# Performance work log

Measured on AMD Instinct MI355X. Metric: run time of the kernel, lower is better.

The kernel has to match this reference:

```python
import jax, jax.numpy as jnp
import numpy as np

N_NODES = 50000
N_EDGES = 600000
N_GRAPHS = 500


def gcn_conv(x, src, dst, W, b, n_nodes):
    # PyG GCNConv: add self-loops, symmetric normalization D^-1/2 (A+I) D^-1/2, then XW + b
    h = x @ W  # [N, F_out]
    loop = jnp.arange(n_nodes)
    s = jnp.concatenate([src, loop])
    d = jnp.concatenate([dst, loop])
    deg = jax.ops.segment_sum(jnp.ones_like(d, dtype=h.dtype), d, num_segments=n_nodes)
    dinv = jnp.where(deg > 0, jax.lax.rsqrt(jnp.maximum(deg, 1.0)), 0.0)
    norm = dinv[s] * dinv[d]  # [E+N]
    msg = h[s] * norm[:, None]  # gather + scale
    out = jax.ops.segment_sum(msg, d, num_segments=n_nodes)  # scatter-add
    return out + b


def setup_inputs() -> dict:
    key = jax.random.key(0)
    ks = jax.random.split(key, 12)
    F_in, H, Hf, D_out = 128, 128, 64, 1
    x = jax.random.normal(ks[0], (N_NODES, F_in), dtype=jnp.float32)
    edge_index = jax.random.randint(ks[1], (2, N_EDGES), 0, N_NODES, dtype=jnp.int64)
    batch = jnp.sort(jax.random.randint(ks[2], (N_NODES,), 0, N_GRAPHS, dtype=jnp.int64))
    def glorot(k, shape):
        lim = np.sqrt(6.0 / (shape[0] + shape[1]))
        return jax.random.uniform(k, shape, jnp.float32, -lim, lim)
    return {
        "x": x, "edge_index": edge_index, "batch": batch,
        "W1": glorot(ks[3], (F_in, H)), "b1": jnp.zeros((H,), jnp.float32),
        "W2": glorot(ks[4], (H, H)), "b2": jnp.zeros((H,), jnp.float32),
        "W3": glorot(ks[5], (H, H)), "b3": jnp.zeros((H,), jnp.float32),
        "Wf1": glorot(ks[6], (H, Hf)), "bf1": jnp.zeros((Hf,), jnp.float32),
        "Wf2": glorot(ks[7], (Hf, D_out)), "bf2": jnp.zeros((D_out,), jnp.float32),
    }


def reference(x, edge_index, batch, W1, b1, W2, b2, W3, b3, Wf1, bf1, Wf2, bf2):
    src, dst = edge_index[0], edge_index[1]
    n = x.shape[0]
    h = jax.nn.relu(gcn_conv(x, src, dst, W1, b1, n))
    h = jax.nn.relu(gcn_conv(h, src, dst, W2, b2, n))
    h = jax.nn.relu(gcn_conv(h, src, dst, W3, b3, n))
    # global_mean_pool: segment mean over graphs
    sums = jax.ops.segment_sum(h, batch, num_segments=N_GRAPHS)
    cnts = jax.ops.segment_sum(jnp.ones((n,), h.dtype), batch, num_segments=N_GRAPHS)
    hg = sums / jnp.maximum(cnts, 1.0)[:, None]  # [G, 128]
    h = jax.nn.relu(hg @ Wf1 + bf1)
    return h @ Wf2 + bf2
```

## Files before the change

### kernel.cpp

```cpp
#include <hip/hip_runtime.h>

#define N_NODES 50000
#define N_EDGES 600000
#define N_GRAPHS 500
#define F 128

typedef short bf16x8 __attribute__((ext_vector_type(8)));
typedef float f32x4 __attribute__((ext_vector_type(4)));
union U4H8 { uint4 u; bf16x8 h; };

__device__ inline unsigned pk_bf16(float a, float b) {
    unsigned ua = __float_as_uint(a), ub = __float_as_uint(b);
    ua = (ua + 0x7fffu + ((ua >> 16) & 1u)) >> 16;
    ub = (ub + 0x7fffu + ((ub >> 16) & 1u)) >> 16;
    return ua | (ub << 16);
}
__device__ inline float bf16_rnd(float x) {
    unsigned u = __float_as_uint(x);
    u = (u + 0x7fffu + ((u >> 16) & 1u)) & 0xffff0000u;
    return __uint_as_float(u);
}
__device__ inline unsigned short bf16_1(float a) {
    unsigned ua = __float_as_uint(a);
    return (unsigned short)((ua + 0x7fffu + ((ua >> 16) & 1u)) >> 16);
}
#define BF_LO(u) __uint_as_float((u) << 16)
#define BF_HI(u) __uint_as_float((u) & 0xffff0000u)

#define G_CVT  3125
#define G_HIST 2344
#define G_PREPW 24
#define G_BND  196

__global__ __launch_bounds__(256) void k_prep(const float* __restrict__ x, unsigned short* __restrict__ xb,
                                              const int* __restrict__ dst, int* __restrict__ cnt,
                                              int* __restrict__ rnk,
                                              const float* __restrict__ W1, const float* __restrict__ W2,
                                              const float* __restrict__ W3,
                                              uint4* __restrict__ Whi, uint4* __restrict__ Wlo,
                                              const int* __restrict__ batch, int* __restrict__ gs) {
    int b = blockIdx.x, tid = threadIdx.x;
    if (b < G_CVT) {
        int idx = b * 256 + tid;
        if (idx < N_NODES * F / 8) {
            const float4* xr = (const float4*)(x + (size_t)idx * 8);
            float4 a = xr[0], c = xr[1];
            uint4 o;
            o.x = pk_bf16(a.x, a.y); o.y = pk_bf16(a.z, a.w);
            o.z = pk_bf16(c.x, c.y); o.w = pk_bf16(c.z, c.w);
            ((uint4*)xb)[idx] = o;
        }
    } else if (b < G_CVT + G_HIST) {
        int e = (b - G_CVT) * 256 + tid;
        if (e < N_EDGES) rnk[e] = atomicAdd(&cnt[dst[e]], 1);
    } else if (b < G_CVT + G_HIST + G_PREPW) {
        int idx = (b - G_CVT - G_HIST) * 256 + tid;
        int layer = idx >> 11;
        const float* W = (layer == 0) ? W1 : (layer == 1) ? W2 : W3;
        int t = idx & 2047;
        int lane = t & 63, sc = t >> 6;
        int s = sc >> 3, c = sc & 7;
        int q = lane >> 4, m = lane & 15;
        int k0 = 32 * s + 8 * q, n0 = 16 * c + m;
        float w[8], h[8];
        #pragma unroll
        for (int j = 0; j < 8; ++j) {
            w[j] = W[(k0 + j) * F + n0];
            h[j] = bf16_rnd(w[j]);
        }
        uint4 uh, ul;
        uh.x = pk_bf16(h[0], h[1]); uh.y = pk_bf16(h[2], h[3]);
        uh.z = pk_bf16(h[4], h[5]); uh.w = pk_bf16(h[6], h[7]);
        ul.x = pk_bf16(w[0] - h[0], w[1] - h[1]); ul.y = pk_bf16(w[2] - h[2], w[3] - h[3]);
        ul.z = pk_bf16(w[4] - h[4], w[5] - h[5]); ul.w = pk_bf16(w[6] - h[6], w[7] - h[7]);
        Whi[idx] = uh;
        Wlo[idx] = ul;
    } else {
        int i = (b - G_CVT - G_HIST - G_PREPW) * 256 + tid;
        if (i < N_NODES) {
            int bi = batch[i];
            if (i == 0) {
                for (int g = 0; g <= bi; ++g) gs[g] = 0;
            } else {
                int bp = batch[i - 1];
                for (int g = bp + 1; g <= bi; ++g) gs[g] = i;
            }
            if (i == N_NODES - 1) {
                for (int g = bi + 1; g <= N_GRAPHS; ++g) gs[g] = N_NODES;
            }
        }
    }
}

__global__ __launch_bounds__(256) void k_scan1(const int* __restrict__ cnt, int* __restrict__ row_ptr,
                                               int* __restrict__ blksums, float* __restrict__ dinv,
                                               int* __restrict__ dh, int n) {
    __shared__ int s[256];
    __shared__ int dhl[64];
    int tid = threadIdx.x;
    int i = blockIdx.x * 256 + tid;
    if (tid < 64) dhl[tid] = 0;
    int v = (i < n) ? cnt[i] : 0;
    if (i < n) dinv[i] = rsqrtf((float)(v + 1));
    s[tid] = v;
    __syncthreads();
    if (i < n) atomicAdd(&dhl[v < 63 ? v : 63], 1);
    for (int off = 1; off < 256; off <<= 1) {
        int t = (tid >= off) ? s[tid - off] : 0;
        __syncthreads();
        s[tid] += t;
        __syncthreads();
    }
    if (i < n) row_ptr[i] = s[tid] - v;
    if (tid == 255) blksums[blockIdx.x] = s[255];
    __syncthreads();
    if (tid < 64 && dhl[tid] > 0) atomicAdd(&dh[tid], dhl[tid]);
}

__global__ __launch_bounds__(256) void k_scan23(int* __restrict__ row_ptr, const int* __restrict__ blksums,
                                                const int* __restrict__ dh, int* __restrict__ dhoff,
                                                int* __restrict__ dcur, int n, int ne) {
    __shared__ int s[256];
    int tid = threadIdx.x;
    s[tid] = (tid < (int)blockIdx.x) ? blksums[tid] : 0;
    __syncthreads();
    for (int off = 128; off > 0; off >>= 1) {
        if (tid < off) s[tid] += s[tid + off];
        __syncthreads();
    }
    int base = s[0];
    int i = blockIdx.x * 256 + tid;
    if (i < n) row_ptr[i] += base;
    if (i == 0) row_ptr[n] = ne;
    if (blockIdx.x == 0 && tid < 64) {
        int v = dh[tid];
        int x = v;
        #pragma unroll
        for (int off = 1; off < 64; off <<= 1) {
            int t = __shfl_up(x, off, 64);
            if (tid >= off) x += t;
        }
        dhoff[tid] = x - v;
        dcur[tid] = 0;
    }
}

#define G_FILL 2344
#define G_PLACE 196
__global__ __launch_bounds__(256) void k_fill(const int* __restrict__ src, const int* __restrict__ dst,
                                              const int* __restrict__ row_ptr, const int* __restrict__ rnk,
                                              int* __restrict__ esrc,
                                              const int* __restrict__ dhoff, int* __restrict__ dcur,
                                              int* __restrict__ perm, int ne) {
    __shared__ int lh[64];
    __shared__ int lbase[64];
    int b = blockIdx.x, tid = threadIdx.x;
    if (b < G_FILL) {
        int e = b * 256 + tid;
        if (e < ne) {
            int d = dst[e];
            esrc[row_ptr[d] + rnk[e]] = src[e];
        }
    } else {
        int i = (b - G_FILL) * 256 + tid;
        if (tid < 64) lh[tid] = 0;
        __syncthreads();
        int deg = 0, rank = 0;
        bool valid = (i < N_NODES);
        if (valid) {
            deg = row_ptr[i + 1] - row_ptr[i];
            if (deg > 63) deg = 63;
            rank = atomicAdd(&lh[deg], 1);
        }
        __syncthreads();
        if (tid < 64 && lh[tid] > 0)
            lbase[tid] = atomicAdd(&dcur[tid], lh[tid]);
        __syncthreads();
        if (valid) perm[dhoff[deg] + lbase[deg] + rank] = i;
    }
}

#define TN 32
#define GP2 136
#define CAPG 32
__global__ __launch_bounds__(256) void k_fused(const int* __restrict__ row_ptr,
                                               const int* __restrict__ esrc,
                                               const float* __restrict__ dinv,
                                               const int* __restrict__ perm,
                                               const unsigned short* __restrict__ Hin,
                                               const uint4* __restrict__ Whi,
                                               const uint4* __restrict__ Wlo,
                                               const float* __restrict__ bias,
                                               unsigned short* __restrict__ Hout, int n) {
    __shared__ unsigned short Gb[TN * GP2];
    __shared__ uint2 eLg[TN][CAPG];
    __shared__ int nodeL[TN], begL[TN], endL[TN];
    __shared__ float ddl[TN];
    int tid = threadIdx.x;
    int d0 = blockIdx.x * TN;
    int grp = tid >> 4, sub = tid & 15;

    if (tid < TN) {
        int slot = d0 + tid;
        int node = (slot < n) ? perm[slot] : -1;
        nodeL[tid] = node;
        if (node >= 0) {
            begL[tid] = row_ptr[node];
            endL[tid] = row_ptr[node + 1];
            ddl[tid] = dinv[node];
        } else {
            begL[tid] = 0; endL[tid] = 0; ddl[tid] = 0.f;
        }
    }
    __syncthreads();

    #pragma unroll 1
    for (int n2 = 0; n2 < 2; ++n2) {
        int gi = grp + 16 * n2;
        int node = nodeL[gi];
        int beg = begL[gi], end = endL[gi];
        int deg = end - beg;
        float dd = ddl[gi];

        int degc = deg < CAPG ? deg : CAPG;
        for (int i = sub; i < degc; i += 16) {
            int s = esrc[beg + i];
            eLg[gi][i] = make_uint2((unsigned)s, (unsigned)__float_as_int(dinv[s]));
        }

        float4 accL = make_float4(0.f, 0.f, 0.f, 0.f);
        float4 accH = make_float4(0.f, 0.f, 0.f, 0.f);
        if (node >= 0) {
            uint4 srow = ((const uint4*)(Hin + (size_t)node * F))[sub];
            float ws = dd * dd;
            accL.x = BF_LO(srow.x) * ws;
            accL.y = BF_HI(srow.x) * ws;
            accL.z = BF_LO(srow.y) * ws;
            accL.w = BF_HI(srow.y) * ws;
            accH.x = BF_LO(srow.z) * ws;
            accH.y = BF_HI(srow.z) * ws;
            accH.z = BF_LO(srow.w) * ws;
            accH.w = BF_HI(srow.w) * ws;
            for (int c = 0; c < deg; c += 8) {
                int sjs[8];
                #pragma unroll
                for (int j = 0; j < 8; ++j) {
                    int e = c + j;
                    int sj = node;
                    if (e < deg) sj = (e < CAPG) ? (int)eLg[gi][e].x
                                                 : esrc[beg + e];
                    sjs[j] = sj;
                }
                uint4 rows[8];
                #pragma unroll
                for (int j = 0; j < 8; ++j)
                    rows[j] = ((const uint4*)(Hin + (size_t)sjs[j] * F))[sub];
                #pragma unroll
                for (int j = 0; j < 8; ++j) {
                    int e = c + j;
                    float wj = 0.f;
                    if (e < deg) {
                        float dv = (e < CAPG) ? __uint_as_float(eLg[gi][e].y)
                                              : dinv[sjs[j]];
                        wj = dv * dd;
                    }
                    accL.x = fmaf(BF_LO(rows[j].x), wj, accL.x);
                    accL.y = fmaf(BF_HI(rows[j].x), wj, accL.y);
                    accL.z = fmaf(BF_LO(rows[j].y), wj, accL.z);
                    accL.w = fmaf(BF_HI(rows[j].y), wj, accL.w);
                    accH.x = fmaf(BF_LO(rows[j].z), wj, accH.x);
                    accH.y = fmaf(BF_HI(rows[j].z), wj, accH.y);
                    accH.z = fmaf(BF_LO(rows[j].w), wj, accH.z);
                    accH.w = fmaf(BF_HI(rows[j].w), wj, accH.w);
                }
            }
        }
        {
            uint4 o;
            o.x = pk_bf16(accL.x, accL.y);
            o.y = pk_bf16(accL.z, accL.w);
            o.z = pk_bf16(accH.x, accH.y);
            o.w = pk_bf16(accH.z, accH.w);
            *(uint4*)&Gb[gi * GP2 + 8 * sub] = o;
        }
    }
    __syncthreads();

    int wave = tid >> 6, lane = tid & 63;
    int q = lane >> 4, m = lane & 15;
    f32x4 acc0[2], acc1[2];
    acc0[0] = (f32x4){0.f, 0.f, 0.f, 0.f};
    acc0[1] = (f32x4){0.f, 0.f, 0.f, 0.f};
    acc1[0] = (f32x4){0.f, 0.f, 0.f, 0.f};
    acc1[1] = (f32x4){0.f, 0.f, 0.f, 0.f};
    #pragma unroll
    for (int s = 0; s < 4; ++s) {
        U4H8 a0, a1;
        a0.u = *(const uint4*)&Gb[m * GP2 + 32 * s + 8 * q];
        a1.u = *(const uint4*)&Gb[(m + 16) * GP2 + 32 * s + 8 * q];
        #pragma unroll
        for (int cc = 0; cc < 2; ++cc) {
            int c = wave * 2 + cc;
            U4H8 bh, bl;
            bh.u = Whi[(s * 8 + c) * 64 + lane];
            bl.u = Wlo[(s * 8 + c) * 64 + lane];
            acc0[cc] = __builtin_amdgcn_mfma_f32_16x16x32_bf16(a0.h, bh.h, acc0[cc], 0, 0, 0);
            acc0[cc] = __builtin_amdgcn_mfma_f32_16x16x32_bf16(a0.h, bl.h, acc0[cc], 0, 0, 0);
            acc1[cc] = __builtin_amdgcn_mfma_f32_16x16x32_bf16(a1.h, bh.h, acc1[cc], 0, 0, 0);
            acc1[cc] = __builtin_amdgcn_mfma_f32_16x16x32_bf16(a1.h, bl.h, acc1[cc], 0, 0, 0);
        }
    }
    __syncthreads();

    #pragma unroll
    for (int cc = 0; cc < 2; ++cc) {
        int c = wave * 2 + cc;
        float bb = bias[16 * c + m];
        #pragma unroll
        for (int r = 0; r < 4; ++r) {
            Gb[(4 * q + r) * GP2 + 16 * c + m] = bf16_1(fmaxf(acc0[cc][r] + bb, 0.f));
            Gb[(16 + 4 * q + r) * GP2 + 16 * c + m] = bf16_1(fmaxf(acc1[cc][r] + bb, 0.f));
        }
    }
    __syncthreads();
    {
        int row = tid >> 4, c8 = tid & 15;
        #pragma unroll
        for (int rr = 0; rr < 2; ++rr) {
            int r2 = row + 16 * rr;
            int onode = nodeL[r2];
            if (onode >= 0) {
                uint4 o = *(const uint4*)&Gb[r2 * GP2 + c8 * 8];
                ((uint4*)(Hout + (size_t)onode * F))[c8] = o;
            }
        }
    }
}

__global__ __launch_bounds__(256) void k_pool_fc(const unsigned short* __restrict__ Hb,
                                                 const int* __restrict__ gs,
                                                 const float* __restrict__ Wf1,
                                                 const float* __restrict__ bf1,
                                                 const float* __restrict__ Wf2,
                                                 const float* __restrict__ bf2,
                                                 float* __restrict__ out) {
    int g = blockIdx.x;
    int tid = threadIdx.x;
    int start = gs[g], end = gs[g + 1];

    __shared__ float hs[4][F];
    __shared__ float hg[F];
    int wv = tid >> 6, lane = tid & 63;
    int half = lane >> 5, sub = lane & 31;
    float4 a = make_float4(0.f, 0.f, 0.f, 0.f);
    for (int i = start + wv * 2 + half; i < end; i += 8) {
        uint2 v = ((const uint2*)(Hb + (size_t)i * F))[sub];
        a.x += BF_LO(v.x); a.y += BF_HI(v.x);
        a.z += BF_LO(v.y); a.w += BF_HI(v.y);
    }
    a.x += __shfl_xor(a.x, 32, 64);
    a.y += __shfl_xor(a.y, 32, 64);
    a.z += __shfl_xor(a.z, 32, 64);
    a.w += __shfl_xor(a.w, 32, 64);
    if (half == 0) ((float4*)hs[wv])[sub] = a;
    __syncthreads();
    if (tid < F) {
        float inv = 1.0f / (float)((end - start) > 0 ? (end - start) : 1);
        hg[tid] = (hs[0][tid] + hs[1][tid] + hs[2][tid] + hs[3][tid]) * inv;
    }
    __syncthreads();
    if (tid < 64) {
        float acc = bf1[tid];
        #pragma unroll 4
        for (int f = 0; f < F; ++f) acc = fmaf(hg[f], Wf1[f * 64 + tid], acc);
        float v = fmaxf(acc, 0.f) * Wf2[tid];
        #pragma unroll
        for (int off = 32; off > 0; off >>= 1) v += __shfl_down(v, off, 64);
        if (tid == 0) out[g] = v + bf2[0];
    }
}

extern "C" void kernel_launch(void* const* d_in, const int* in_sizes, int n_in,
                              void* d_out, int out_size, void* d_ws, size_t ws_size,
                              hipStream_t stream) {
    const float* x    = (const float*)d_in[0];
    const int* eidx   = (const int*)d_in[1];
    const int* batch  = (const int*)d_in[2];
    const float* W1   = (const float*)d_in[3];
    const float* b1   = (const float*)d_in[4];
    const float* W2   = (const float*)d_in[5];
    const float* b2   = (const float*)d_in[6];
    const float* W3   = (const float*)d_in[7];
    const float* b3   = (const float*)d_in[8];
    const float* Wf1  = (const float*)d_in[9];
    const float* bf1  = (const float*)d_in[10];
    const float* Wf2  = (const float*)d_in[11];
    const float* bf2  = (const float*)d_in[12];
    float* out = (float*)d_out;

    const int* src = eidx;
    const int* dst = eidx + N_EDGES;

    char* p = (char*)d_ws;
    unsigned short* Xb  = (unsigned short*)p;  p += (size_t)N_NODES * F * 2;
    unsigned short* H1  = (unsigned short*)p;  p += (size_t)N_NODES * F * 2;
    unsigned short* H2  = (unsigned short*)p;  p += (size_t)N_NODES * F * 2;
    unsigned short* H3  = (unsigned short*)p;  p += (size_t)N_NODES * F * 2;
    int* esrc   = (int*)p;     p += (size_t)N_EDGES * sizeof(int);
    int* rnk    = (int*)p;     p += (size_t)N_EDGES * sizeof(int);
    uint4* Whi  = (uint4*)p;   p += (size_t)3 * 2048 * sizeof(uint4);
    uint4* Wlo  = (uint4*)p;   p += (size_t)3 * 2048 * sizeof(uint4);
    float* dinv = (float*)p;   p += (size_t)N_NODES * sizeof(float);
    int* cnt     = (int*)p;    p += (size_t)N_NODES * sizeof(int);
    int* dh      = (int*)p;    p += 64 * sizeof(int);
    int* row_ptr = (int*)p;    p += (size_t)(N_NODES + 1) * sizeof(int);
    int* blksums = (int*)p;    p += 256 * sizeof(int);
    int* gs      = (int*)p;    p += (size_t)(N_GRAPHS + 1) * sizeof(int);
    int* dhoff   = (int*)p;    p += 64 * sizeof(int);
    int* dcur    = (int*)p;    p += 64 * sizeof(int);
    int* perm    = (int*)p;    p += (size_t)N_NODES * sizeof(int);

    dim3 b256(256);
    int gNodes = (N_NODES + 255) / 256;
    int gFused = (N_NODES + TN - 1) / TN;

    hipMemsetAsync(cnt, 0, ((size_t)N_NODES + 64) * sizeof(int), stream);
    k_prep<<<G_CVT + G_HIST + G_PREPW + G_BND, b256, 0, stream>>>(x, Xb, dst, cnt, rnk, W1, W2, W3,
                                                                  Whi, Wlo, batch, gs);

    k_scan1<<<gNodes, b256, 0, stream>>>(cnt, row_ptr, blksums, dinv, dh, N_NODES);
    k_scan23<<<gNodes, b256, 0, stream>>>(row_ptr, blksums, dh, dhoff, dcur, N_NODES, N_EDGES);
    k_fill<<<G_FILL + G_PLACE, b256, 0, stream>>>(src, dst, row_ptr, rnk, esrc,
                                                  dhoff, dcur, perm, N_EDGES);

    k_fused<<<gFused, b256, 0, stream>>>(row_ptr, esrc, dinv, perm, Xb, Whi,        Wlo,        b1, H1, N_NODES);
    k_fused<<<gFused, b256, 0, stream>>>(row_ptr, esrc, dinv, perm, H1, Whi + 2048, Wlo + 2048, b2, H2, N_NODES);
    k_fused<<<gFused, b256, 0, stream>>>(row_ptr, esrc, dinv, perm, H2, Whi + 4096, Wlo + 4096, b3, H3, N_NODES);

    k_pool_fc<<<N_GRAPHS, b256, 0, stream>>>(H3, gs, Wf1, bf1, Wf2, bf2, out);
}
```

Before: 241.7 us.

## Interleave two destination nodes per thread group with software-pipelined neighbor gathers

The aggregation stage now handles both destination nodes assigned to a 16-thread group at the same time instead of one after another. It double-buffers the 8-row neighbor gathers so the next batch of loads is issued while the current batch is accumulated. Edges beyond the shared-memory cap of 32 go through a separate scalar tail loop. The aim is more memory-level parallelism to hide gather latency, at the cost of higher register pressure (two 8×uint4 buffers and two accumulator sets), which may reduce occupancy.

```diff
diff --git a/kernel.cpp b/kernel.cpp
--- a/kernel.cpp
+++ b/kernel.cpp
@@ -183,6 +183,33 @@
 #define TN 32
 #define GP2 136
 #define CAPG 32
+
+__device__ __forceinline__ void issue8(uint4* buf, const uint2* eRow, int dc, int abase,
+                                       int c, const unsigned short* __restrict__ Hin, int sub) {
+    #pragma unroll
+    for (int j = 0; j < 8; ++j) {
+        int e = c + j;
+        int sj = (e < dc) ? (int)eRow[e].x : abase;
+        buf[j] = ((const uint4*)(Hin + (size_t)sj * F))[sub];
+    }
+}
+__device__ __forceinline__ void fma8(const uint4* buf, const uint2* eRow, int dc, float dd,
+                                     int c, float4& aL, float4& aH) {
+    #pragma unroll
+    for (int j = 0; j < 8; ++j) {
+        int e = c + j;
+        float wj = (e < dc) ? __uint_as_float(eRow[e].y) * dd : 0.f;
+        aL.x = fmaf(BF_LO(buf[j].x), wj, aL.x);
+        aL.y = fmaf(BF_HI(buf[j].x), wj, aL.y);
+        aL.z = fmaf(BF_LO(buf[j].y), wj, aL.z);
+        aL.w = fmaf(BF_HI(buf[j].y), wj, aL.w);
+        aH.x = fmaf(BF_LO(buf[j].z), wj, aH.x);
+        aH.y = fmaf(BF_HI(buf[j].z), wj, aH.y);
+        aH.z = fmaf(BF_LO(buf[j].w), wj, aH.z);
+        aH.w = fmaf(BF_HI(buf[j].w), wj, aH.w);
+    }
+}
+
 __global__ __launch_bounds__(256) void k_fused(const int* __restrict__ row_ptr,
                                                const int* __restrict__ esrc,
                                                const float* __restrict__ dinv,
@@ -214,75 +241,86 @@
     }
     __syncthreads();
 
-    #pragma unroll 1
-    for (int n2 = 0; n2 < 2; ++n2) {
-        int gi = grp + 16 * n2;
-        int node = nodeL[gi];
-        int beg = begL[gi], end = endL[gi];
-        int deg = end - beg;
-        float dd = ddl[gi];
-
-        int degc = deg < CAPG ? deg : CAPG;
-        for (int i = sub; i < degc; i += 16) {
-            int s = esrc[beg + i];
-            eLg[gi][i] = make_uint2((unsigned)s, (unsigned)__float_as_int(dinv[s]));
-        }
-
-        float4 accL = make_float4(0.f, 0.f, 0.f, 0.f);
-        float4 accH = make_float4(0.f, 0.f, 0.f, 0.f);
-        if (node >= 0) {
-            uint4 srow = ((const uint4*)(Hin + (size_t)node * F))[sub];
-            float ws = dd * dd;
-            accL.x = BF_LO(srow.x) * ws;
-            accL.y = BF_HI(srow.x) * ws;
-            accL.z = BF_LO(srow.y) * ws;
-            accL.w = BF_HI(srow.y) * ws;
-            accH.x = BF_LO(srow.z) * ws;
-            accH.y = BF_HI(srow.z) * ws;
-            accH.z = BF_LO(srow.w) * ws;
-            accH.w = BF_HI(srow.w) * ws;
-            for (int c = 0; c < deg; c += 8) {
-                int sjs[8];
-                #pragma unroll
-                for (int j = 0; j < 8; ++j) {
-                    int e = c + j;
-                    int sj = node;
-                    if (e < deg) sj = (e < CAPG) ? (int)eLg[gi][e].x
-                                                 : esrc[beg + e];
-                    sjs[j] = sj;
-                }
-                uint4 rows[8];
-                #pragma unroll
-                for (int j = 0; j < 8; ++j)
-                    rows[j] = ((const uint4*)(Hin + (size_t)sjs[j] * F))[sub];
-                #pragma unroll
-                for (int j = 0; j < 8; ++j) {
-                    int e = c + j;
-                    float wj = 0.f;
-                    if (e < deg) {
-                        float dv = (e < CAPG) ? __uint_as_float(eLg[gi][e].y)
-                                              : dinv[sjs[j]];
-                        wj = dv * dd;
-                    }
-                    accL.x = fmaf(BF_LO(rows[j].x), wj, accL.x);
-                    accL.y = fmaf(BF_HI(rows[j].x), wj, accL.y);
-                    accL.z = fmaf(BF_LO(rows[j].y), wj, accL.z);
-                    accL.w = fmaf(BF_HI(rows[j].y), wj, accL.w);
-                    accH.x = fmaf(BF_LO(rows[j].z), wj, accH.x);
-                    accH.y = fmaf(BF_HI(rows[j].z), wj, accH.y);
-                    accH.z = fmaf(BF_LO(rows[j].w), wj, accH.z);
-                    accH.w = fmaf(BF_HI(rows[j].w), wj, accH.w);
-                }
+    {
+        int gi0 = grp, gi1 = grp + 16;
+        int node0 = nodeL[gi0], node1 = nodeL[gi1];
+        int beg0 = begL[gi0], deg0 = endL[gi0] - beg0;
+        int beg1 = begL[gi1], deg1 = endL[gi1] - beg1;
+        float dd0 = ddl[gi0], dd1 = ddl[gi1];
+        int a0 = node0 >= 0 ? node0 : 0;
+        int a1 = node1 >= 0 ? node1 : 0;
+
+        uint4 s0 = ((const uint4*)(Hin + (size_t)a0 * F))[sub];
+        uint4 s1 = ((const uint4*)(Hin + (size_t)a1 * F))[sub];
+
+        int dc0 = deg0 < CAPG ? deg0 : CAPG;
+        int dc1 = deg1 < CAPG ? deg1 : CAPG;
+        for (int i = sub; i < dc0; i += 16) {
+            int s = esrc[beg0 + i];
+            eLg[gi0][i] = make_uint2((unsigned)s, (unsigned)__float_as_int(dinv[s]));
+        }
+        for (int i = sub; i < dc1; i += 16) {
+            int s = esrc[beg1 + i];
+            eLg[gi1][i] = make_uint2((unsigned)s, (unsigned)__float_as_int(dinv[s]));
+        }
+        const uint2* eR0 = &eLg[gi0][0];
+        const uint2* eR1 = &eLg[gi1][0];
+
+        int nb0 = (dc0 + 7) >> 3, nb1 = (dc1 + 7) >> 3;
+        uint4 bufA[8], bufB[8];
+        if (nb0) issue8(bufA, eR0, dc0, a0, 0, Hin, sub);
+        if (nb1) issue8(bufB, eR1, dc1, a1, 0, Hin, sub);
+
+        float ws0 = node0 >= 0 ? dd0 * dd0 : 0.f;
+        float ws1 = node1 >= 0 ? dd1 * dd1 : 0.f;
+        float4 aL0, aH0, aL1, aH1;
+        aL0.x = BF_LO(s0.x) * ws0; aL0.y = BF_HI(s0.x) * ws0;
+        aL0.z = BF_LO(s0.y) * ws0; aL0.w = BF_HI(s0.y) * ws0;
+        aH0.x = BF_LO(s0.z) * ws0; aH0.y = BF_HI(s0.z) * ws0;
+        aH0.z = BF_LO(s0.w) * ws0; aH0.w = BF_HI(s0.w) * ws0;
+        aL1.x = BF_LO(s1.x) * ws1; aL1.y = BF_HI(s1.x) * ws1;
+        aL1.z = BF_LO(s1.y) * ws1; aL1.w = BF_HI(s1.y) * ws1;
+        aH1.x = BF_LO(s1.z) * ws1; aH1.y = BF_HI(s1.z) * ws1;
+        aH1.z = BF_LO(s1.w) * ws1; aH1.w = BF_HI(s1.w) * ws1;
+
+        int nbm = nb0 > nb1 ? nb0 : nb1;
+        #pragma unroll 1
+        for (int t = 0; t < nbm; ++t) {
+            if (t < nb0) {
+                fma8(bufA, eR0, dc0, dd0, 8 * t, aL0, aH0);
+                if (t + 1 < nb0) issue8(bufA, eR0, dc0, a0, 8 * (t + 1), Hin, sub);
             }
-        }
-        {
-            uint4 o;
-            o.x = pk_bf16(accL.x, accL.y);
-            o.y = pk_bf16(accL.z, accL.w);
-            o.z = pk_bf16(accH.x, accH.y);
-            o.w = pk_bf16(accH.z, accH.w);
-            *(uint4*)&Gb[gi * GP2 + 8 * sub] = o;
-        }
+            if (t < nb1) {
+                fma8(bufB, eR1, dc1, dd1, 8 * t, aL1, aH1);
+                if (t + 1 < nb1) issue8(bufB, eR1, dc1, a1, 8 * (t + 1), Hin, sub);
+            }
+        }
+        for (int e = CAPG; e < deg0; ++e) {
+            int sj = esrc[beg0 + e];
+            float wj = dinv[sj] * dd0;
+            uint4 r = ((const uint4*)(Hin + (size_t)sj * F))[sub];
+            aL0.x = fmaf(BF_LO(r.x), wj, aL0.x); aL0.y = fmaf(BF_HI(r.x), wj, aL0.y);
+            aL0.z = fmaf(BF_LO(r.y), wj, aL0.z); aL0.w = fmaf(BF_HI(r.y), wj, aL0.w);
+            aH0.x = fmaf(BF_LO(r.z), wj, aH0.x); aH0.y = fmaf(BF_HI(r.z), wj, aH0.y);
+            aH0.z = fmaf(BF_LO(r.w), wj, aH0.z); aH0.w = fmaf(BF_HI(r.w), wj, aH0.w);
+        }
+        for (int e = CAPG; e < deg1; ++e) {
+            int sj = esrc[beg1 + e];
+            float wj = dinv[sj] * dd1;
+            uint4 r = ((const uint4*)(Hin + (size_t)sj * F))[sub];
+            aL1.x = fmaf(BF_LO(r.x), wj, aL1.x); aL1.y = fmaf(BF_HI(r.x), wj, aL1.y);
+            aL1.z = fmaf(BF_LO(r.y), wj, aL1.z); aL1.w = fmaf(BF_HI(r.y), wj, aL1.w);
+            aH1.x = fmaf(BF_LO(r.z), wj, aH1.x); aH1.y = fmaf(BF_HI(r.z), wj, aH1.y);
+            aH1.z = fmaf(BF_LO(r.w), wj, aH1.z); aH1.w = fmaf(BF_HI(r.w), wj, aH1.w);
+        }
+
+        uint4 o0, o1;
+        o0.x = pk_bf16(aL0.x, aL0.y); o0.y = pk_bf16(aL0.z, aL0.w);
+        o0.z = pk_bf16(aH0.x, aH0.y); o0.w = pk_bf16(aH0.z, aH0.w);
+        o1.x = pk_bf16(aL1.x, aL1.y); o1.y = pk_bf16(aL1.z, aL1.w);
+        o1.z = pk_bf16(aH1.x, aH1.y); o1.w = pk_bf16(aH1.z, aH1.w);
+        *(uint4*)&Gb[gi0 * GP2 + 8 * sub] = o0;
+        *(uint4*)&Gb[gi1 * GP2 + 8 * sub] = o1;
     }
     __syncthreads();
 
```

Measured after the change: 265.0 us. 1.1x slower.

## Split fused GCN layer into column-chunked aggregation and matmul kernels

Applied to the files above, without the earlier changes.

Stores node features in a chunked layout (8 column chunks of 16 bf16 per node), so each aggregation block gathers only one 32-byte chunk per neighbor. The intent is a per-chunk working set (about 1.6 MB) small enough to stay in cache during the random gathers. Aggregation is split out of the fused kernel into a separate k_agg kernel that writes an intermediate Agg buffer, which k_mm then multiplies by W. The cost is an extra kernel launch and a write and read of the intermediate per layer, plus reloading esrc and dinv once per chunk, and the gathers become narrow 4-byte loads per lane.

```diff
diff --git a/kernel.cpp b/kernel.cpp
--- a/kernel.cpp
+++ b/kernel.cpp
@@ -26,6 +26,7 @@
 }
 #define BF_LO(u) __uint_as_float((u) << 16)
 #define BF_HI(u) __uint_as_float((u) & 0xffff0000u)
+
 
 #define G_CVT  3125
 #define G_HIST 2344
@@ -44,11 +45,13 @@
         int idx = b * 256 + tid;
         if (idx < N_NODES * F / 8) {
             const float4* xr = (const float4*)(x + (size_t)idx * 8);
-            float4 a = xr[0], c = xr[1];
+            float4 a = xr[0], c4 = xr[1];
             uint4 o;
             o.x = pk_bf16(a.x, a.y); o.y = pk_bf16(a.z, a.w);
-            o.z = pk_bf16(c.x, c.y); o.w = pk_bf16(c.z, c.w);
-            ((uint4*)xb)[idx] = o;
+            o.z = pk_bf16(c4.x, c4.y); o.w = pk_bf16(c4.z, c4.w);
+            int node = idx >> 4, q = idx & 15;
+            int c = q >> 1, half = q & 1;
+            ((uint4*)xb)[((size_t)c * N_NODES + node) * 2 + half] = o;
         }
     } else if (b < G_CVT + G_HIST) {
         int e = (b - G_CVT) * 256 + tid;
@@ -180,109 +183,74 @@
     }
 }
 
+#define AB 32
+__global__ __launch_bounds__(256) void k_agg(const int* __restrict__ row_ptr,
+                                             const int* __restrict__ esrc,
+                                             const float* __restrict__ dinv,
+                                             const int* __restrict__ perm,
+                                             const unsigned short* __restrict__ Hb,
+                                             unsigned short* __restrict__ Agg, int n) {
+    int bid = blockIdx.x;
+    int c = bid & 7;
+    int nb = bid >> 3;
+    int tid = threadIdx.x;
+    int g = tid >> 3, l = tid & 7;
+    int slot = nb * AB + g;
+    int node = (slot < n) ? perm[slot] : -1;
+    if (node < 0) return;
+    int beg = row_ptr[node], end = row_ptr[node + 1];
+    float dd = dinv[node];
+    const unsigned* base = (const unsigned*)(Hb + (size_t)c * N_NODES * 16);
+    unsigned sr = base[(size_t)node * 8 + l];
+    float ws = dd * dd;
+    float ax = BF_LO(sr) * ws, ay = BF_HI(sr) * ws;
+    int e = beg;
+    for (; e + 4 <= end; e += 4) {
+        int s0 = esrc[e], s1 = esrc[e + 1], s2 = esrc[e + 2], s3 = esrc[e + 3];
+        float w0 = dinv[s0] * dd, w1 = dinv[s1] * dd, w2 = dinv[s2] * dd, w3 = dinv[s3] * dd;
+        unsigned r0 = base[(size_t)s0 * 8 + l];
+        unsigned r1 = base[(size_t)s1 * 8 + l];
+        unsigned r2 = base[(size_t)s2 * 8 + l];
+        unsigned r3 = base[(size_t)s3 * 8 + l];
+        ax = fmaf(BF_LO(r0), w0, ax); ay = fmaf(BF_HI(r0), w0, ay);
+        ax = fmaf(BF_LO(r1), w1, ax); ay = fmaf(BF_HI(r1), w1, ay);
+        ax = fmaf(BF_LO(r2), w2, ax); ay = fmaf(BF_HI(r2), w2, ay);
+        ax = fmaf(BF_LO(r3), w3, ax); ay = fmaf(BF_HI(r3), w3, ay);
+    }
+    for (; e < end; ++e) {
+        int s0 = esrc[e];
+        float w0 = dinv[s0] * dd;
+        unsigned r0 = base[(size_t)s0 * 8 + l];
+        ax = fmaf(BF_LO(r0), w0, ax); ay = fmaf(BF_HI(r0), w0, ay);
+    }
+    ((unsigned*)Agg)[(size_t)c * N_NODES * 8 + (size_t)node * 8 + l] = pk_bf16(ax, ay);
+}
+
 #define TN 32
 #define GP2 136
-#define CAPG 32
-__global__ __launch_bounds__(256) void k_fused(const int* __restrict__ row_ptr,
-                                               const int* __restrict__ esrc,
-                                               const float* __restrict__ dinv,
-                                               const int* __restrict__ perm,
-                                               const unsigned short* __restrict__ Hin,
-                                               const uint4* __restrict__ Whi,
-                                               const uint4* __restrict__ Wlo,
-                                               const float* __restrict__ bias,
-                                               unsigned short* __restrict__ Hout, int n) {
+__global__ __launch_bounds__(256) void k_mm(const int* __restrict__ perm,
+                                            const unsigned short* __restrict__ Agg,
+                                            const uint4* __restrict__ Whi,
+                                            const uint4* __restrict__ Wlo,
+                                            const float* __restrict__ bias,
+                                            unsigned short* __restrict__ Hout, int n) {
     __shared__ unsigned short Gb[TN * GP2];
-    __shared__ uint2 eLg[TN][CAPG];
-    __shared__ int nodeL[TN], begL[TN], endL[TN];
-    __shared__ float ddl[TN];
+    __shared__ int nodeL[TN];
     int tid = threadIdx.x;
     int d0 = blockIdx.x * TN;
-    int grp = tid >> 4, sub = tid & 15;
-
-    if (tid < TN) {
-        int slot = d0 + tid;
-        int node = (slot < n) ? perm[slot] : -1;
-        nodeL[tid] = node;
+    if (tid < TN) nodeL[tid] = (d0 + tid < n) ? perm[d0 + tid] : -1;
+    __syncthreads();
+
+    {
+        int c = tid >> 5, r = tid & 31;
+        int node = nodeL[r];
+        uint4 v0 = make_uint4(0, 0, 0, 0), v1 = v0;
         if (node >= 0) {
-            begL[tid] = row_ptr[node];
-            endL[tid] = row_ptr[node + 1];
-            ddl[tid] = dinv[node];
-        } else {
-            begL[tid] = 0; endL[tid] = 0; ddl[tid] = 0.f;
-        }
-    }
-    __syncthreads();
-
-    #pragma unroll 1
-    for (int n2 = 0; n2 < 2; ++n2) {
-        int gi = grp + 16 * n2;
-        int node = nodeL[gi];
-        int beg = begL[gi], end = endL[gi];
-        int deg = end - beg;
-        float dd = ddl[gi];
-
-        int degc = deg < CAPG ? deg : CAPG;
-        for (int i = sub; i < degc; i += 16) {
-            int s = esrc[beg + i];
-            eLg[gi][i] = make_uint2((unsigned)s, (unsigned)__float_as_int(dinv[s]));
-        }
-
-        float4 accL = make_float4(0.f, 0.f, 0.f, 0.f);
-        float4 accH = make_float4(0.f, 0.f, 0.f, 0.f);
-        if (node >= 0) {
-            uint4 srow = ((const uint4*)(Hin + (size_t)node * F))[sub];
-            float ws = dd * dd;
-            accL.x = BF_LO(srow.x) * ws;
-            accL.y = BF_HI(srow.x) * ws;
-            accL.z = BF_LO(srow.y) * ws;
-            accL.w = BF_HI(srow.y) * ws;
-            accH.x = BF_LO(srow.z) * ws;
-            accH.y = BF_HI(srow.z) * ws;
-            accH.z = BF_LO(srow.w) * ws;
-            accH.w = BF_HI(srow.w) * ws;
-            for (int c = 0; c < deg; c += 8) {
-                int sjs[8];
-                #pragma unroll
-                for (int j = 0; j < 8; ++j) {
-                    int e = c + j;
-                    int sj = node;
-                    if (e < deg) sj = (e < CAPG) ? (int)eLg[gi][e].x
-                                                 : esrc[beg + e];
-                    sjs[j] = sj;
-                }
-                uint4 rows[8];
-                #pragma unroll
-                for (int j = 0; j < 8; ++j)
-                    rows[j] = ((const uint4*)(Hin + (size_t)sjs[j] * F))[sub];
-                #pragma unroll
-                for (int j = 0; j < 8; ++j) {
-                    int e = c + j;
-                    float wj = 0.f;
-                    if (e < deg) {
-                        float dv = (e < CAPG) ? __uint_as_float(eLg[gi][e].y)
-                                              : dinv[sjs[j]];
-                        wj = dv * dd;
-                    }
-                    accL.x = fmaf(BF_LO(rows[j].x), wj, accL.x);
-                    accL.y = fmaf(BF_HI(rows[j].x), wj, accL.y);
-                    accL.z = fmaf(BF_LO(rows[j].y), wj, accL.z);
-                    accL.w = fmaf(BF_HI(rows[j].y), wj, accL.w);
-                    accH.x = fmaf(BF_LO(rows[j].z), wj, accH.x);
-                    accH.y = fmaf(BF_HI(rows[j].z), wj, accH.y);
-                    accH.z = fmaf(BF_LO(rows[j].w), wj, accH.z);
-                    accH.w = fmaf(BF_HI(rows[j].w), wj, accH.w);
-                }
-            }
-        }
-        {
-            uint4 o;
-            o.x = pk_bf16(accL.x, accL.y);
-            o.y = pk_bf16(accL.z, accL.w);
-            o.z = pk_bf16(accH.x, accH.y);
-            o.w = pk_bf16(accH.z, accH.w);
-            *(uint4*)&Gb[gi * GP2 + 8 * sub] = o;
-        }
+            const uint4* srcp = (const uint4*)(Agg + ((size_t)c * N_NODES + node) * 16);
+            v0 = srcp[0]; v1 = srcp[1];
+        }
+        *(uint4*)&Gb[r * GP2 + c * 16] = v0;
+        *(uint4*)&Gb[r * GP2 + c * 16 + 8] = v1;
     }
     __syncthreads();
 
@@ -324,15 +292,13 @@
     }
     __syncthreads();
     {
-        int row = tid >> 4, c8 = tid & 15;
-        #pragma unroll
-        for (int rr = 0; rr < 2; ++rr) {
-            int r2 = row + 16 * rr;
-            int onode = nodeL[r2];
-            if (onode >= 0) {
-                uint4 o = *(const uint4*)&Gb[r2 * GP2 + c8 * 8];
-                ((uint4*)(Hout + (size_t)onode * F))[c8] = o;
-            }
+        int c = tid >> 5, r = tid & 31;
+        int node = nodeL[r];
+        if (node >= 0) {
+            uint4 v0 = *(const uint4*)&Gb[r * GP2 + c * 16];
+            uint4 v1 = *(const uint4*)&Gb[r * GP2 + c * 16 + 8];
+            uint4* dstp = (uint4*)(Hout + ((size_t)c * N_NODES + node) * 16);
+            dstp[0] = v0; dstp[1] = v1;
         }
     }
 }
@@ -352,9 +318,10 @@
     __shared__ float hg[F];
     int wv = tid >> 6, lane = tid & 63;
     int half = lane >> 5, sub = lane & 31;
+    int c = sub >> 2, w = sub & 3;
     float4 a = make_float4(0.f, 0.f, 0.f, 0.f);
     for (int i = start + wv * 2 + half; i < end; i += 8) {
-        uint2 v = ((const uint2*)(Hb + (size_t)i * F))[sub];
+        uint2 v = *(const uint2*)((const char*)Hb + ((size_t)c * N_NODES + i) * 32 + w * 8);
         a.x += BF_LO(v.x); a.y += BF_HI(v.x);
         a.z += BF_LO(v.y); a.w += BF_HI(v.y);
     }
@@ -406,6 +373,7 @@
     unsigned short* H1  = (unsigned short*)p;  p += (size_t)N_NODES * F * 2;
     unsigned short* H2  = (unsigned short*)p;  p += (size_t)N_NODES * F * 2;
     unsigned short* H3  = (unsigned short*)p;  p += (size_t)N_NODES * F * 2;
+    unsigned short* Agg = (unsigned short*)p;  p += (size_t)N_NODES * F * 2;
     int* esrc   = (int*)p;     p += (size_t)N_EDGES * sizeof(int);
     int* rnk    = (int*)p;     p += (size_t)N_EDGES * sizeof(int);
     uint4* Whi  = (uint4*)p;   p += (size_t)3 * 2048 * sizeof(uint4);
@@ -422,7 +390,8 @@
 
     dim3 b256(256);
     int gNodes = (N_NODES + 255) / 256;
-    int gFused = (N_NODES + TN - 1) / TN;
+    int gTile  = (N_NODES + TN - 1) / TN;
+    int gAgg   = 8 * ((N_NODES + AB - 1) / AB);
 
     hipMemsetAsync(cnt, 0, ((size_t)N_NODES + 64) * sizeof(int), stream);
     k_prep<<<G_CVT + G_HIST + G_PREPW + G_BND, b256, 0, stream>>>(x, Xb, dst, cnt, rnk, W1, W2, W3,
@@ -433,9 +402,12 @@
     k_fill<<<G_FILL + G_PLACE, b256, 0, stream>>>(src, dst, row_ptr, rnk, esrc,
                                                   dhoff, dcur, perm, N_EDGES);
 
-    k_fused<<<gFused, b256, 0, stream>>>(row_ptr, esrc, dinv, perm, Xb, Whi,        Wlo,        b1, H1, N_NODES);
-    k_fused<<<gFused, b256, 0, stream>>>(row_ptr, esrc, dinv, perm, H1, Whi + 2048, Wlo + 2048, b2, H2, N_NODES);
-    k_fused<<<gFused, b256, 0, stream>>>(row_ptr, esrc, dinv, perm, H2, Whi + 4096, Wlo + 4096, b3, H3, N_NODES);
+    k_agg<<<gAgg, b256, 0, stream>>>(row_ptr, esrc, dinv, perm, Xb, Agg, N_NODES);
+    k_mm <<<gTile, b256, 0, stream>>>(perm, Agg, Whi,        Wlo,        b1, H1, N_NODES);
+    k_agg<<<gAgg, b256, 0, stream>>>(row_ptr, esrc, dinv, perm, H1, Agg, N_NODES);
+    k_mm <<<gTile, b256, 0, stream>>>(perm, Agg, Whi + 2048, Wlo + 2048, b2, H2, N_NODES);
+    k_agg<<<gAgg, b256, 0, stream>>>(row_ptr, esrc, dinv, perm, H2, Agg, N_NODES);
+    k_mm <<<gTile, b256, 0, stream>>>(perm, Agg, Whi + 4096, Wlo + 4096, b3, H3, N_NODES);
 
     k_pool_fc<<<N_GRAPHS, b256, 0, stream>>>(H3, gs, Wf1, bf1, Wf2, bf2, out);
 }
```

Result: slower. 379.3 us (+56.9%).
